# Kernel optimization log

Measured on AMD Instinct MI355X. Metric: run time of the kernel, lower is better.

## Reference

```python
import jax, jax.numpy as jnp
import numpy as np


def setup_inputs() -> dict:
    key = jax.random.key(0)
    k1, k2 = jax.random.split(key)
    B, S, D, K = 8, 2048, 512, 8192
    x = jax.random.normal(k1, (B, S, D), dtype=jnp.float32)
    codebook = jax.random.normal(k2, (K, D), dtype=jnp.float32)
    return {"x": x, "codebook": codebook}


def reference(x, codebook):
    # x: [B, S, D], codebook: [K, D]
    B, S, D = x.shape
    flat_x = x.reshape(-1, D)                      # [N, D], N = B*S
    distances = (
        jnp.sum(flat_x * flat_x, axis=1, keepdims=True)
        - 2.0 * jnp.matmul(flat_x, codebook.T)
        + jnp.sum(codebook * codebook, axis=1)
    )
    encoding_indices = jnp.argmin(distances, axis=1)  # [N]
    quantized = codebook[encoding_indices]            # [N, D] embedding lookup
    return quantized.reshape(x.shape)                 # [B, S, D]
```

## Files before the change

### kernel.cpp

```cpp
#include <hip/hip_runtime.h>


#define MROWS 16384
#define KCB   8192
#define DDIM  512
#define BM 256
#define BN 256
#define BK 64
#define NKT (DDIM / BK)
#define NTILES (KCB / 128)
#define MARGIN 8.0f

typedef unsigned short u16;
typedef unsigned int uint;
typedef __attribute__((ext_vector_type(8))) short bf16x8;
typedef __attribute__((ext_vector_type(4))) float f32x4;

__device__ inline u16 f2bf(float f) {
  unsigned int u = __float_as_uint(f);
  u += 0x7FFFu + ((u >> 16) & 1u);
  return (u16)(u >> 16);
}

__device__ inline void gload16(const void* g, void* l) {
  __builtin_amdgcn_global_load_lds((const __attribute__((address_space(1))) void*)g,
                                   (__attribute__((address_space(3))) void*)l,
                                   16, 0, 0);
}

__device__ inline double shfl_xor_dbl(double v, int m) {
  long long l = __double_as_longlong(v);
  int lo = (int)(l & 0xffffffffLL), hi = (int)(l >> 32);
  lo = __shfl_xor(lo, m, 64);
  hi = __shfl_xor(hi, m, 64);
  return __longlong_as_double(((long long)hi << 32) | (unsigned long long)(unsigned int)lo);
}

__device__ inline float keyval(uint k) {
  uint u = k & 0xFFFFFF80u;
  uint bits = (u & 0x80000000u) ? (u & 0x7FFFFFFFu) : ~u;
  return __uint_as_float(bits);
}


__global__ __launch_bounds__(256) void k_conv_x(const float* __restrict__ x,
                                                u16* __restrict__ xb) {
  size_t i = ((size_t)blockIdx.x * 256 + threadIdx.x) * 8;
  float4 a = *(const float4*)(x + i);
  float4 b = *(const float4*)(x + i + 4);
  union { u16 s[8]; uint4 v; } u;
  u.s[0]=f2bf(a.x); u.s[1]=f2bf(a.y); u.s[2]=f2bf(a.z); u.s[3]=f2bf(a.w);
  u.s[4]=f2bf(b.x); u.s[5]=f2bf(b.y); u.s[6]=f2bf(b.z); u.s[7]=f2bf(b.w);
  *(uint4*)(xb + i) = u.v;
}

__global__ __launch_bounds__(256) void k_conv_cb(const float* __restrict__ cb,
                                                 u16* __restrict__ cbb,
                                                 float* __restrict__ cnorm) {
  int k = blockIdx.x * 4 + (threadIdx.x >> 6);
  int lane = threadIdx.x & 63;
  size_t base = (size_t)k * DDIM + lane * 8;
  float4 a = *(const float4*)(cb + base);
  float4 b = *(const float4*)(cb + base + 4);
  union { u16 s[8]; uint4 v; } u;
  u.s[0]=f2bf(a.x); u.s[1]=f2bf(a.y); u.s[2]=f2bf(a.z); u.s[3]=f2bf(a.w);
  u.s[4]=f2bf(b.x); u.s[5]=f2bf(b.y); u.s[6]=f2bf(b.z); u.s[7]=f2bf(b.w);
  *(uint4*)(cbb + base) = u.v;
  float s = a.x*a.x + a.y*a.y + a.z*a.z + a.w*a.w
          + b.x*b.x + b.y*b.y + b.z*b.z + b.w*b.w;
  #pragma unroll
  for (int m = 1; m < 64; m <<= 1) s += __shfl_xor(s, m, 64);
  if (lane == 0) cnorm[k] = s;
}


__global__ __launch_bounds__(512, 2) void k_gemm_min(
    const u16* __restrict__ Xbf, const u16* __restrict__ Cbf,
    const float* __restrict__ cnorm, uint2* __restrict__ stats)
{
  extern __shared__ u16 lds[];

  int bid = blockIdx.x;
  int xcd = bid & 7;
  int j   = bid >> 3;
  int mTile = xcd * 8 + (j & 7);
  int nTile = j >> 3;
  int rowBase = mTile * BM;
  int colBase = nTile * BN;

  int tid = threadIdx.x;
  int lane = tid & 63;
  int wv = tid >> 6;
  int wr = wv >> 2;
  int wc = wv & 3;
  int grp = lane >> 4;
  int l15 = lane & 15;

  const u16 *srcX[4], *srcC[4];
  #pragma unroll
  for (int i = 0; i < 4; ++i) {
    int f = i * 512 + tid;
    int r = f >> 3;
    int p = f & 7;
    int gc = (p ^ (r & 7)) << 3;
    srcX[i] = Xbf + (size_t)(rowBase + r) * DDIM + gc;
    srcC[i] = Cbf + (size_t)(colBase + r) * DDIM + gc;
  }

  f32x4 acc[8][4];
  #pragma unroll
  for (int mi = 0; mi < 8; ++mi)
    #pragma unroll
    for (int ni = 0; ni < 4; ++ni)
      acc[mi][ni] = (f32x4){0.f, 0.f, 0.f, 0.f};

#define STAGE(cur_, kt_)                                                     \
  {                                                                          \
    u16* Xd = lds + (cur_) * 16384;                                          \
    u16* Cd = lds + 32768 + (cur_) * 16384;                                  \
    _Pragma("unroll")                                                        \
    for (int i = 0; i < 4; ++i) {                                            \
      gload16(srcX[i] + (kt_) * BK, (void*)(Xd + (i * 512 + wv * 64) * 8));  \
      gload16(srcC[i] + (kt_) * BK, (void*)(Cd + (i * 512 + wv * 64) * 8));  \
    }                                                                        \
  }

  STAGE(0, 0);
  STAGE(1, 1);
  __syncthreads();

  int cur = 0;
  for (int kt = 0; kt < NKT; ++kt) {
    const u16* Xb = lds + cur * 16384;
    const u16* Cs = lds + 32768 + cur * 16384;
    #pragma unroll
    for (int ks = 0; ks < 2; ++ks) {
      bf16x8 xF[4];
      #pragma unroll
      for (int ni = 0; ni < 4; ++ni) {
        int rX = wc * 64 + ni * 16 + l15;
        xF[ni] = *(const bf16x8*)&Xb[rX * BK + (((ks * 4 + grp) ^ (rX & 7)) << 3)];
      }
      #pragma unroll
      for (int mi = 0; mi < 8; ++mi) {
        int rC = wr * 128 + mi * 16 + l15;
        bf16x8 cF = *(const bf16x8*)&Cs[rC * BK + (((ks * 4 + grp) ^ (rC & 7)) << 3)];
        #pragma unroll
        for (int ni = 0; ni < 4; ++ni)
          acc[mi][ni] = __builtin_amdgcn_mfma_f32_16x16x32_bf16(cF, xF[ni], acc[mi][ni], 0, 0, 0);
      }
    }
    __syncthreads();
    if (kt + 2 < NKT) STAGE(cur, kt + 2);
    cur ^= 1;
  }
#undef STAGE

#define INS(st1, st2, st3, kx)                                     \
  { uint kk_ = (kx);                                               \
    bool lt1 = kk_ < st1, lt2 = kk_ < st2, lt3 = kk_ < st3;        \
    st3 = lt3 ? (lt2 ? st2 : kk_) : st3;                           \
    st2 = lt2 ? (lt1 ? st1 : kk_) : st2;                           \
    st1 = lt1 ? kk_ : st1; }

  uint t1[4], t2[4], t3[4];
  #pragma unroll
  for (int ni = 0; ni < 4; ++ni) { t1[ni] = 0xFFFFFFFFu; t2[ni] = 0xFFFFFFFFu; t3[ni] = 0xFFFFFFFFu; }

  #pragma unroll
  for (int mi = 0; mi < 8; ++mi) {
    float cnv[4];
    *(float4*)cnv = *(const float4*)&cnorm[colBase + wr * 128 + mi * 16 + grp * 4];
    #pragma unroll
    for (int ni = 0; ni < 4; ++ni) {
      #pragma unroll
      for (int rg = 0; rg < 4; ++rg) {
        float v = cnv[rg] - 2.0f * acc[mi][ni][rg];
        uint u = __float_as_uint(v);
        u = ((int)u < 0) ? ~u : (u | 0x80000000u);
        uint key = (u & 0xFFFFFF80u) | (uint)(mi * 16 + grp * 4 + rg);
        INS(t1[ni], t2[ni], t3[ni], key);
      }
    }
  }
  #pragma unroll
  for (int ni = 0; ni < 4; ++ni) {
    #pragma unroll
    for (int mk = 16; mk <= 32; mk <<= 1) {
      uint o1 = (uint)__shfl_xor((int)t1[ni], mk, 64);
      uint o2 = (uint)__shfl_xor((int)t2[ni], mk, 64);
      uint o3 = (uint)__shfl_xor((int)t3[ni], mk, 64);
      INS(t1[ni], t2[ni], t3[ni], o1);
      INS(t1[ni], t2[ni], t3[ni], o2);
      INS(t1[ni], t2[ni], t3[ni], o3);
    }
  }
#undef INS
  if (grp == 0) {
    #pragma unroll
    for (int ni = 0; ni < 4; ++ni) {
      float v1 = keyval(t1[ni]), v2 = keyval(t2[ni]), v3 = keyval(t3[ni]);
      uint i1 = t1[ni] & 127u, i2 = t2[ni] & 127u;
      uint d2 = min(255u, (uint)((v2 - v1) * 4.0f));
      uint d3 = min(255u, (uint)((v3 - v1) * 4.0f));
      uint2 st;
      st.x = __float_as_uint(v1);
      st.y = i1 | (i2 << 7) | (d2 << 14) | (d3 << 22);
      int xrow = rowBase + wc * 64 + ni * 16 + l15;
      stats[(size_t)xrow * NTILES + nTile * 2 + wr] = st;
    }
  }
}


__device__ inline void eval64(const float4& xa, const float4& xb,
                              const float* __restrict__ cb, int col,
                              double& best, int& bi, int lane) {
  const float* cr = cb + (size_t)col * DDIM + lane * 8;
  float4 ca = *(const float4*)cr;
  float4 cv = *(const float4*)(cr + 4);
  double s = 0.0, d;
  d = (double)xa.x - (double)ca.x; s += d*d;
  d = (double)xa.y - (double)ca.y; s += d*d;
  d = (double)xa.z - (double)ca.z; s += d*d;
  d = (double)xa.w - (double)ca.w; s += d*d;
  d = (double)xb.x - (double)cv.x; s += d*d;
  d = (double)xb.y - (double)cv.y; s += d*d;
  d = (double)xb.z - (double)cv.z; s += d*d;
  d = (double)xb.w - (double)cv.w; s += d*d;
  #pragma unroll
  for (int m = 1; m < 64; m <<= 1) s += shfl_xor_dbl(s, m);
  if (s < best || (s == best && col < bi)) { best = s; bi = col; }
}

__global__ __launch_bounds__(256) void k_refine(
    const float* __restrict__ x, const float* __restrict__ cb,
    const float* __restrict__ cnorm, const uint2* __restrict__ stats,
    unsigned int* __restrict__ bestOut)
{
  int n = blockIdx.x * 4 + (threadIdx.x >> 6);
  int lane = threadIdx.x & 63;
  uint2 st = stats[(size_t)n * NTILES + lane];
  float m1 = __uint_as_float(st.x);
  int   i1 = st.y & 127, i2 = (st.y >> 7) & 127;
  float m2 = m1 + ((st.y >> 14) & 255u) * 0.25f;
  float m3 = m1 + ((st.y >> 22) & 255u) * 0.25f;
  float g = m1;
  #pragma unroll
  for (int m = 1; m < 64; m <<= 1) g = fminf(g, __shfl_xor(g, m, 64));
  float T = g + MARGIN;
  unsigned long long q1 = __ballot(m1 <= T);
  unsigned long long q2 = __ballot(m2 <= T);
  unsigned long long qr = __ballot(m3 <= T);

  const float* xr = x + (size_t)n * DDIM;
  float4 xa = *(const float4*)(xr + lane * 8);
  float4 xb = *(const float4*)(xr + lane * 8 + 4);

  double best = 1e300;
  int bi = 0x7fffffff;

  while (q1) {
    int t = __ffsll(q1) - 1; q1 &= q1 - 1;
    int col = t * 128 + __shfl(i1, t, 64);
    eval64(xa, xb, cb, col, best, bi, lane);
  }
  while (q2) {
    int t = __ffsll(q2) - 1; q2 &= q2 - 1;
    int col = t * 128 + __shfl(i2, t, 64);
    eval64(xa, xb, cb, col, best, bi, lane);
  }
  while (qr) {
    int t = __ffsll(qr) - 1; qr &= qr - 1;
    for (int c2 = 0; c2 < 128; ++c2) {
      int col2 = t * 128 + c2;
      const float* cr = cb + (size_t)col2 * DDIM + lane * 8;
      float4 ca = *(const float4*)cr;
      float4 cv = *(const float4*)(cr + 4);
      float p = xa.x*ca.x + xa.y*ca.y + xa.z*ca.z + xa.w*ca.w
              + xb.x*cv.x + xb.y*cv.y + xb.z*cv.z + xb.w*cv.w;
      #pragma unroll
      for (int m = 1; m < 64; m <<= 1) p += __shfl_xor(p, m, 64);
      float s32 = cnorm[col2] - 2.0f * p;
      if (s32 <= T) {
        double s = 0.0, dd;
        dd = (double)xa.x - (double)ca.x; s += dd*dd;
        dd = (double)xa.y - (double)ca.y; s += dd*dd;
        dd = (double)xa.z - (double)ca.z; s += dd*dd;
        dd = (double)xa.w - (double)ca.w; s += dd*dd;
        dd = (double)xb.x - (double)cv.x; s += dd*dd;
        dd = (double)xb.y - (double)cv.y; s += dd*dd;
        dd = (double)xb.z - (double)cv.z; s += dd*dd;
        dd = (double)xb.w - (double)cv.w; s += dd*dd;
        #pragma unroll
        for (int m = 1; m < 64; m <<= 1) s += shfl_xor_dbl(s, m);
        if (s < best || (s == best && col2 < bi)) { best = s; bi = col2; }
      }
    }
  }
  if (lane == 0) bestOut[n] = (unsigned int)bi;
}


__global__ __launch_bounds__(256) void k_gather(const float* __restrict__ cb,
                                                const unsigned int* __restrict__ bestIdx,
                                                float* __restrict__ out) {
  int n = blockIdx.x * 4 + (threadIdx.x >> 6);
  int lane = threadIdx.x & 63;
  unsigned int b = bestIdx[n];
  const float4* s = (const float4*)(cb + (size_t)b * DDIM);
  float4* dp = (float4*)(out + (size_t)n * DDIM);
  dp[lane * 2]     = s[lane * 2];
  dp[lane * 2 + 1] = s[lane * 2 + 1];
}


extern "C" void kernel_launch(void* const* d_in, const int* in_sizes, int n_in,
                              void* d_out, int out_size, void* d_ws, size_t ws_size,
                              hipStream_t stream) {
  const float* x  = (const float*)d_in[0];
  const float* cb = (const float*)d_in[1];
  float* out = (float*)d_out;

  char* ob = (char*)d_out;
  u16*   Xbf   = (u16*)ob;
  u16*   Cbf   = (u16*)(ob + 16ull * 1024 * 1024);
  uint2* stats = (uint2*)(ob + 24ull * 1024 * 1024);

  char* wsb = (char*)d_ws;
  float* cnorm = (float*)wsb;
  unsigned int* bestIdx = (unsigned int*)(wsb + 32 * 1024);

  (void)hipFuncSetAttribute((const void*)k_gemm_min,
                            hipFuncAttributeMaxDynamicSharedMemorySize, 131072);

  k_conv_x  <<<4096, 256, 0, stream>>>(x, Xbf);
  k_conv_cb <<<2048, 256, 0, stream>>>(cb, Cbf, cnorm);
  k_gemm_min<<<2048, 512, 131072, stream>>>(Xbf, Cbf, cnorm, stats);
  k_refine  <<<4096, 256, 0, stream>>>(x, cb, cnorm, stats, bestIdx);
  k_gather  <<<4096, 256, 0, stream>>>(cb, bestIdx, out);
}
```

Before: 267.6 us.

## Restructure GEMM main loop into fine-grained phased pipeline with manual waitcnt

Replaces the double-buffered K-loop (two syncthreads per tile) with an eight-phase schedule per pair of K-tiles. Each phase loads a quarter of the next tile's operands with direct-to-LDS loads, waits on vmcnt by hand, and issues 16 MFMAs at raised wave priority. The LDS layout is split into half-tiles and offsets are precomputed. The goal is finer overlap of global loads, LDS reads and MFMA work, at the cost of fragile hand-written barrier and waitcnt logic that could introduce races.

```diff
diff --git a/kernel.cpp b/kernel.cpp
--- a/kernel.cpp
+++ b/kernel.cpp
@@ -4,10 +4,7 @@
 #define MROWS 16384
 #define KCB   8192
 #define DDIM  512
-#define BM 256
-#define BN 256
-#define BK 64
-#define NKT (DDIM / BK)
+#define NKT   8
 #define NTILES (KCB / 128)
 #define MARGIN 8.0f
 
@@ -78,15 +75,15 @@
     const u16* __restrict__ Xbf, const u16* __restrict__ Cbf,
     const float* __restrict__ cnorm, uint2* __restrict__ stats)
 {
-  extern __shared__ u16 lds[];
+  extern __shared__ __align__(16) u16 lds[];
 
   int bid = blockIdx.x;
   int xcd = bid & 7;
   int j   = bid >> 3;
   int mTile = xcd * 8 + (j & 7);
   int nTile = j >> 3;
-  int rowBase = mTile * BM;
-  int colBase = nTile * BN;
+  int rowBase = mTile * 256;
+  int colBase = nTile * 256;
 
   int tid = threadIdx.x;
   int lane = tid & 63;
@@ -96,16 +93,18 @@
   int grp = lane >> 4;
   int l15 = lane & 15;
 
-  const u16 *srcX[4], *srcC[4];
-  #pragma unroll
-  for (int i = 0; i < 4; ++i) {
-    int f = i * 512 + tid;
-    int r = f >> 3;
-    int p = f & 7;
-    int gc = (p ^ (r & 7)) << 3;
-    srcX[i] = Xbf + (size_t)(rowBase + r) * DDIM + gc;
-    srcC[i] = Cbf + (size_t)(colBase + r) * DDIM + gc;
-  }
+  const int rr = tid >> 3;
+  const int pc = (tid & 7) ^ (rr & 7);
+  const u16* pA = Cbf + (size_t)(colBase + rr) * DDIM + pc * 8;
+  const u16* pB = Xbf + (size_t)(rowBase + rr) * DDIM + pc * 8;
+
+  const int m7 = l15 & 7;
+  const int ch0 = (grp ^ m7);
+  const int ch1 = ch0 ^ 4;
+  const int cOff0 = wr * 4096 + l15 * 64 + ch0 * 8;
+  const int cOff1 = wr * 4096 + l15 * 64 + ch1 * 8;
+  const int xOff0 = wc * 4096 + l15 * 64 + ch0 * 8;
+  const int xOff1 = wc * 4096 + l15 * 64 + ch1 * 8;
 
   f32x4 acc[8][4];
   #pragma unroll
@@ -114,47 +113,72 @@
     for (int ni = 0; ni < 4; ++ni)
       acc[mi][ni] = (f32x4){0.f, 0.f, 0.f, 0.f};
 
-#define STAGE(cur_, kt_)                                                     \
-  {                                                                          \
-    u16* Xd = lds + (cur_) * 16384;                                          \
-    u16* Cd = lds + 32768 + (cur_) * 16384;                                  \
-    _Pragma("unroll")                                                        \
-    for (int i = 0; i < 4; ++i) {                                            \
-      gload16(srcX[i] + (kt_) * BK, (void*)(Xd + (i * 512 + wv * 64) * 8));  \
-      gload16(srcC[i] + (kt_) * BK, (void*)(Cd + (i * 512 + wv * 64) * 8));  \
-    }                                                                        \
-  }
-
-  STAGE(0, 0);
-  STAGE(1, 1);
-  __syncthreads();
-
-  int cur = 0;
-  for (int kt = 0; kt < NKT; ++kt) {
-    const u16* Xb = lds + cur * 16384;
-    const u16* Cs = lds + 32768 + cur * 16384;
-    #pragma unroll
-    for (int ks = 0; ks < 2; ++ks) {
-      bf16x8 xF[4];
+  gload16(pB,           (void*)&lds[32768 + tid * 8]);
+  gload16(pB + 32768,   (void*)&lds[32768 + 4096 + tid * 8]);
+  gload16(pB + 65536,   (void*)&lds[32768 + 8192 + tid * 8]);
+  gload16(pB + 98304,   (void*)&lds[32768 + 12288 + tid * 8]);
+  gload16(pA,           (void*)&lds[tid * 8]);
+  gload16(pA + 65536,   (void*)&lds[4096 + tid * 8]);
+  gload16(pA + 32768,   (void*)&lds[8192 + tid * 8]);
+  gload16(pA + 98304,   (void*)&lds[8192 + 4096 + tid * 8]);
+
+  bf16x8 xF[4];
+
+  #pragma unroll
+  for (int it = 0; it < 4; ++it) {
+    #pragma unroll
+    for (int ph = 0; ph < 8; ++ph) {
+      const int b  = ph >> 2;
+      const int s  = ph & 3;
+      const int h  = s & 1;
+      const int ks = s >> 1;
+      const int tauS = 2 * it + 1 + (ph >> 2);
+      const int bS = (ph < 4) ? 1 : 0;
+
+      if ((ph & 2) == 0) {
+        if (it == 3 && ph == 5) { asm volatile("s_waitcnt vmcnt(0)" ::: "memory"); }
+        else                    { asm volatile("s_waitcnt vmcnt(2)" ::: "memory"); }
+      }
+      __builtin_amdgcn_s_barrier();
+      __builtin_amdgcn_sched_barrier(0);
+
+      bf16x8 cF[4];
       #pragma unroll
-      for (int ni = 0; ni < 4; ++ni) {
-        int rX = wc * 64 + ni * 16 + l15;
-        xF[ni] = *(const bf16x8*)&Xb[rX * BK + (((ks * 4 + grp) ^ (rX & 7)) << 3)];
-      }
-      #pragma unroll
-      for (int mi = 0; mi < 8; ++mi) {
-        int rC = wr * 128 + mi * 16 + l15;
-        bf16x8 cF = *(const bf16x8*)&Cs[rC * BK + (((ks * 4 + grp) ^ (rC & 7)) << 3)];
+      for (int q = 0; q < 4; ++q)
+        cF[q] = *(const bf16x8*)&lds[b * 16384 + h * 8192 + q * 1024 + (ks ? cOff1 : cOff0)];
+      if (h == 0) {
         #pragma unroll
         for (int ni = 0; ni < 4; ++ni)
-          acc[mi][ni] = __builtin_amdgcn_mfma_f32_16x16x32_bf16(cF, xF[ni], acc[mi][ni], 0, 0, 0);
-      }
-    }
-    __syncthreads();
-    if (kt + 2 < NKT) STAGE(cur, kt + 2);
-    cur ^= 1;
-  }
-#undef STAGE
+          xF[ni] = *(const bf16x8*)&lds[32768 + b * 16384 + ni * 1024 + (ks ? xOff1 : xOff0)];
+      }
+
+      if (!(it == 3 && ph >= 4)) {
+        if (s < 2) {
+          gload16(pB + s * 65536 + tauS * 64,
+                  (void*)&lds[32768 + bS * 16384 + s * 8192 + tid * 8]);
+          gload16(pB + s * 65536 + 32768 + tauS * 64,
+                  (void*)&lds[32768 + bS * 16384 + s * 8192 + 4096 + tid * 8]);
+        } else {
+          const int ha = s - 2;
+          gload16(pA + ha * 32768 + tauS * 64,
+                  (void*)&lds[bS * 16384 + ha * 8192 + tid * 8]);
+          gload16(pA + ha * 32768 + 65536 + tauS * 64,
+                  (void*)&lds[bS * 16384 + ha * 8192 + 4096 + tid * 8]);
+        }
+      }
+
+      asm volatile("s_waitcnt lgkmcnt(0)" ::: "memory");
+      __builtin_amdgcn_sched_barrier(0);
+      __builtin_amdgcn_s_setprio(1);
+      #pragma unroll
+      for (int q = 0; q < 4; ++q)
+        #pragma unroll
+        for (int ni = 0; ni < 4; ++ni)
+          acc[h * 4 + q][ni] =
+            __builtin_amdgcn_mfma_f32_16x16x32_bf16(cF[q], xF[ni], acc[h * 4 + q][ni], 0, 0, 0);
+      __builtin_amdgcn_s_setprio(0);
+    }
+  }
 
 #define INS(st1, st2, st3, kx)                                     \
   { uint kk_ = (kx);                                               \
```

New measurement: 257.4 us. 3.8% less time.

## Shrink GEMM tile to 128x256 with BK32, raise occupancy, fuse refine+gather

Applied to the files above, without the earlier changes.

Retiles the bf16 distance GEMM from 256x256 with BK=64 to 128 rows by 256 codewords with BK=32. Per-block LDS drops from 128KB to 48KB, so four 512-thread blocks can fit per CU, and wave priority is raised around the MFMA burst. A new LDS cross-wave merge combines the two 64-codeword halves into the existing per-128-column top-3 stats. When the workspace is large enough, stats move to the workspace and refine and gather fuse into one kernel, saving a launch and the index round trip. The smaller tile lowers data reuse per loaded byte and adds a synchronised merge step.

```diff
diff --git a/kernel.cpp b/kernel.cpp
--- a/kernel.cpp
+++ b/kernel.cpp
@@ -4,11 +4,8 @@
 #define MROWS 16384
 #define KCB   8192
 #define DDIM  512
-#define BM 256
-#define BN 256
-#define BK 64
-#define NKT (DDIM / BK)
-#define NTILES (KCB / 128)
+#define NKT   16
+#define NTILES 64
 #define MARGIN 8.0f
 
 typedef unsigned short u16;
@@ -74,55 +71,55 @@
 }
 
 
-__global__ __launch_bounds__(512, 2) void k_gemm_min(
+__global__ __launch_bounds__(512, 4) void k_gemm_min(
     const u16* __restrict__ Xbf, const u16* __restrict__ Cbf,
     const float* __restrict__ cnorm, uint2* __restrict__ stats)
 {
-  extern __shared__ u16 lds[];
+  extern __shared__ __align__(16) u16 lds[];
 
   int bid = blockIdx.x;
   int xcd = bid & 7;
   int j   = bid >> 3;
-  int mTile = xcd * 8 + (j & 7);
-  int nTile = j >> 3;
-  int rowBase = mTile * BM;
-  int colBase = nTile * BN;
+  int mTile = xcd * 16 + (j & 15);
+  int nTile = j >> 4;
+  int rowBase = mTile * 128;
+  int colBase = nTile * 256;
 
   int tid = threadIdx.x;
   int lane = tid & 63;
   int wv = tid >> 6;
-  int wr = wv >> 2;
-  int wc = wv & 3;
+  int wr = wv & 3;
+  int wc = wv >> 2;
   int grp = lane >> 4;
   int l15 = lane & 15;
 
-  const u16 *srcX[4], *srcC[4];
+  const int ar = tid >> 2;
+  const int ac = ((tid & 3) ^ ((ar + (ar >> 2)) & 3)) << 3;
+  const u16* pA = Cbf + (size_t)(colBase + ar) * DDIM + ac;
+  const u16* pB = Xbf + (size_t)(rowBase + ar) * DDIM + ac;
+
+  int offA[4], offX[4];
   #pragma unroll
   for (int i = 0; i < 4; ++i) {
-    int f = i * 512 + tid;
-    int r = f >> 3;
-    int p = f & 7;
-    int gc = (p ^ (r & 7)) << 3;
-    srcX[i] = Xbf + (size_t)(rowBase + r) * DDIM + gc;
-    srcC[i] = Cbf + (size_t)(colBase + r) * DDIM + gc;
-  }
-
-  f32x4 acc[8][4];
-  #pragma unroll
-  for (int mi = 0; mi < 8; ++mi)
+    int rA = wr * 64 + i * 16 + l15;
+    offA[i] = rA * 32 + ((grp ^ ((rA + (rA >> 2)) & 3)) << 3);
+    int rX = wc * 64 + i * 16 + l15;
+    offX[i] = 8192 + rX * 32 + ((grp ^ ((rX + (rX >> 2)) & 3)) << 3);
+  }
+
+  f32x4 acc[4][4];
+  #pragma unroll
+  for (int mi = 0; mi < 4; ++mi)
     #pragma unroll
     for (int ni = 0; ni < 4; ++ni)
       acc[mi][ni] = (f32x4){0.f, 0.f, 0.f, 0.f};
 
-#define STAGE(cur_, kt_)                                                     \
-  {                                                                          \
-    u16* Xd = lds + (cur_) * 16384;                                          \
-    u16* Cd = lds + 32768 + (cur_) * 16384;                                  \
-    _Pragma("unroll")                                                        \
-    for (int i = 0; i < 4; ++i) {                                            \
-      gload16(srcX[i] + (kt_) * BK, (void*)(Xd + (i * 512 + wv * 64) * 8));  \
-      gload16(srcC[i] + (kt_) * BK, (void*)(Cd + (i * 512 + wv * 64) * 8));  \
-    }                                                                        \
+#define STAGE(b_, T)                                                          \
+  {                                                                           \
+    u16* Ad = lds + (b_) * 12288;                                             \
+    gload16(pA + (T) * 32,               (void*)(Ad + tid * 8));              \
+    gload16(pA + 65536 + (T) * 32,       (void*)(Ad + 4096 + tid * 8));       \
+    gload16(pB + (T) * 32,               (void*)(Ad + 8192 + tid * 8));       \
   }
 
   STAGE(0, 0);
@@ -131,25 +128,19 @@
 
   int cur = 0;
   for (int kt = 0; kt < NKT; ++kt) {
-    const u16* Xb = lds + cur * 16384;
-    const u16* Cs = lds + 32768 + cur * 16384;
-    #pragma unroll
-    for (int ks = 0; ks < 2; ++ks) {
-      bf16x8 xF[4];
+    const u16* base = lds + cur * 12288;
+    bf16x8 cF[4], xF[4];
+    #pragma unroll
+    for (int mi = 0; mi < 4; ++mi) cF[mi] = *(const bf16x8*)&base[offA[mi]];
+    #pragma unroll
+    for (int ni = 0; ni < 4; ++ni) xF[ni] = *(const bf16x8*)&base[offX[ni]];
+    __builtin_amdgcn_s_setprio(1);
+    #pragma unroll
+    for (int mi = 0; mi < 4; ++mi)
       #pragma unroll
-      for (int ni = 0; ni < 4; ++ni) {
-        int rX = wc * 64 + ni * 16 + l15;
-        xF[ni] = *(const bf16x8*)&Xb[rX * BK + (((ks * 4 + grp) ^ (rX & 7)) << 3)];
-      }
-      #pragma unroll
-      for (int mi = 0; mi < 8; ++mi) {
-        int rC = wr * 128 + mi * 16 + l15;
-        bf16x8 cF = *(const bf16x8*)&Cs[rC * BK + (((ks * 4 + grp) ^ (rC & 7)) << 3)];
-        #pragma unroll
-        for (int ni = 0; ni < 4; ++ni)
-          acc[mi][ni] = __builtin_amdgcn_mfma_f32_16x16x32_bf16(cF, xF[ni], acc[mi][ni], 0, 0, 0);
-      }
-    }
+      for (int ni = 0; ni < 4; ++ni)
+        acc[mi][ni] = __builtin_amdgcn_mfma_f32_16x16x32_bf16(cF[mi], xF[ni], acc[mi][ni], 0, 0, 0);
+    __builtin_amdgcn_s_setprio(0);
     __syncthreads();
     if (kt + 2 < NKT) STAGE(cur, kt + 2);
     cur ^= 1;
@@ -167,10 +158,11 @@
   #pragma unroll
   for (int ni = 0; ni < 4; ++ni) { t1[ni] = 0xFFFFFFFFu; t2[ni] = 0xFFFFFFFFu; t3[ni] = 0xFFFFFFFFu; }
 
-  #pragma unroll
-  for (int mi = 0; mi < 8; ++mi) {
+  const uint tagBase = (uint)((wr & 1) * 64);
+  #pragma unroll
+  for (int mi = 0; mi < 4; ++mi) {
     float cnv[4];
-    *(float4*)cnv = *(const float4*)&cnorm[colBase + wr * 128 + mi * 16 + grp * 4];
+    *(float4*)cnv = *(const float4*)&cnorm[colBase + wr * 64 + mi * 16 + grp * 4];
     #pragma unroll
     for (int ni = 0; ni < 4; ++ni) {
       #pragma unroll
@@ -178,7 +170,7 @@
         float v = cnv[rg] - 2.0f * acc[mi][ni][rg];
         uint u = __float_as_uint(v);
         u = ((int)u < 0) ? ~u : (u | 0x80000000u);
-        uint key = (u & 0xFFFFFF80u) | (uint)(mi * 16 + grp * 4 + rg);
+        uint key = (u & 0xFFFFFF80u) | (tagBase + (uint)(mi * 16 + grp * 4 + rg));
         INS(t1[ni], t2[ni], t3[ni], key);
       }
     }
@@ -195,21 +187,35 @@
       INS(t1[ni], t2[ni], t3[ni], o3);
     }
   }
+
+  uint* scK = (uint*)lds;
+  if (grp == 0) {
+    #pragma unroll
+    for (int ni = 0; ni < 4; ++ni) {
+      int xloc = wc * 64 + ni * 16 + l15;
+      uint* p = &scK[(wr * 128 + xloc) * 3];
+      p[0] = t1[ni]; p[1] = t2[ni]; p[2] = t3[ni];
+    }
+  }
+  __syncthreads();
+  if (tid < 256) {
+    int xr = tid & 127;
+    int s  = tid >> 7;
+    const uint* pa = &scK[((2 * s) * 128 + xr) * 3];
+    const uint* pb = &scK[((2 * s + 1) * 128 + xr) * 3];
+    uint a1 = pa[0], a2 = pa[1], a3 = pa[2];
+    #pragma unroll
+    for (int z = 0; z < 3; ++z) INS(a1, a2, a3, pb[z]);
+    float v1 = keyval(a1), v2 = keyval(a2), v3 = keyval(a3);
+    uint i1 = a1 & 127u, i2 = a2 & 127u;
+    uint d2 = min(255u, (uint)((v2 - v1) * 4.0f));
+    uint d3 = min(255u, (uint)((v3 - v1) * 4.0f));
+    uint2 st;
+    st.x = __float_as_uint(v1);
+    st.y = i1 | (i2 << 7) | (d2 << 14) | (d3 << 22);
+    stats[(size_t)(rowBase + xr) * NTILES + nTile * 2 + s] = st;
+  }
 #undef INS
-  if (grp == 0) {
-    #pragma unroll
-    for (int ni = 0; ni < 4; ++ni) {
-      float v1 = keyval(t1[ni]), v2 = keyval(t2[ni]), v3 = keyval(t3[ni]);
-      uint i1 = t1[ni] & 127u, i2 = t2[ni] & 127u;
-      uint d2 = min(255u, (uint)((v2 - v1) * 4.0f));
-      uint d3 = min(255u, (uint)((v3 - v1) * 4.0f));
-      uint2 st;
-      st.x = __float_as_uint(v1);
-      st.y = i1 | (i2 << 7) | (d2 << 14) | (d3 << 22);
-      int xrow = rowBase + wc * 64 + ni * 16 + l15;
-      stats[(size_t)xrow * NTILES + nTile * 2 + wr] = st;
-    }
-  }
 }
 
 
@@ -233,13 +239,10 @@
   if (s < best || (s == best && col < bi)) { best = s; bi = col; }
 }
 
-__global__ __launch_bounds__(256) void k_refine(
-    const float* __restrict__ x, const float* __restrict__ cb,
-    const float* __restrict__ cnorm, const uint2* __restrict__ stats,
-    unsigned int* __restrict__ bestOut)
-{
-  int n = blockIdx.x * 4 + (threadIdx.x >> 6);
-  int lane = threadIdx.x & 63;
+__device__ inline int refine_row(int n, int lane,
+                                 const float* __restrict__ x, const float* __restrict__ cb,
+                                 const float* __restrict__ cnorm,
+                                 const uint2* __restrict__ stats) {
   uint2 st = stats[(size_t)n * NTILES + lane];
   float m1 = __uint_as_float(st.x);
   int   i1 = st.y & 127, i2 = (st.y >> 7) & 127;
@@ -298,9 +301,33 @@
       }
     }
   }
+  return bi;
+}
+
+__global__ __launch_bounds__(256) void k_refine(
+    const float* __restrict__ x, const float* __restrict__ cb,
+    const float* __restrict__ cnorm, const uint2* __restrict__ stats,
+    unsigned int* __restrict__ bestOut)
+{
+  int n = blockIdx.x * 4 + (threadIdx.x >> 6);
+  int lane = threadIdx.x & 63;
+  int bi = refine_row(n, lane, x, cb, cnorm, stats);
   if (lane == 0) bestOut[n] = (unsigned int)bi;
 }
 
+__global__ __launch_bounds__(256) void k_refine_gather(
+    const float* __restrict__ x, const float* __restrict__ cb,
+    const float* __restrict__ cnorm, const uint2* __restrict__ stats,
+    float* __restrict__ out)
+{
+  int n = blockIdx.x * 4 + (threadIdx.x >> 6);
+  int lane = threadIdx.x & 63;
+  int bi = refine_row(n, lane, x, cb, cnorm, stats);
+  const float4* s = (const float4*)(cb + (size_t)bi * DDIM);
+  float4* dp = (float4*)(out + (size_t)n * DDIM);
+  dp[lane * 2]     = s[lane * 2];
+  dp[lane * 2 + 1] = s[lane * 2 + 1];
+}
 
 __global__ __launch_bounds__(256) void k_gather(const float* __restrict__ cb,
                                                 const unsigned int* __restrict__ bestIdx,
@@ -323,20 +350,28 @@
   float* out = (float*)d_out;
 
   char* ob = (char*)d_out;
-  u16*   Xbf   = (u16*)ob;
-  u16*   Cbf   = (u16*)(ob + 16ull * 1024 * 1024);
-  uint2* stats = (uint2*)(ob + 24ull * 1024 * 1024);
+  u16* Xbf = (u16*)ob;
+  u16* Cbf = (u16*)(ob + 16ull * 1024 * 1024);
 
   char* wsb = (char*)d_ws;
   float* cnorm = (float*)wsb;
   unsigned int* bestIdx = (unsigned int*)(wsb + 32 * 1024);
 
+  const size_t statsBytes = (size_t)MROWS * NTILES * sizeof(uint2);
+  bool fuse = ws_size >= 96 * 1024 + statsBytes;
+  uint2* stats = fuse ? (uint2*)(wsb + 96 * 1024)
+                      : (uint2*)(ob + 24ull * 1024 * 1024);
+
   (void)hipFuncSetAttribute((const void*)k_gemm_min,
-                            hipFuncAttributeMaxDynamicSharedMemorySize, 131072);
+                            hipFuncAttributeMaxDynamicSharedMemorySize, 49152);
 
   k_conv_x  <<<4096, 256, 0, stream>>>(x, Xbf);
   k_conv_cb <<<2048, 256, 0, stream>>>(cb, Cbf, cnorm);
-  k_gemm_min<<<2048, 512, 131072, stream>>>(Xbf, Cbf, cnorm, stats);
-  k_refine  <<<4096, 256, 0, stream>>>(x, cb, cnorm, stats, bestIdx);
-  k_gather  <<<4096, 256, 0, stream>>>(cb, bestIdx, out);
-}
+  k_gemm_min<<<4096, 512, 49152, stream>>>(Xbf, Cbf, cnorm, stats);
+  if (fuse) {
+    k_refine_gather<<<4096, 256, 0, stream>>>(x, cb, cnorm, stats, out);
+  } else {
+    k_refine<<<4096, 256, 0, stream>>>(x, cb, cnorm, stats, bestIdx);
+    k_gather<<<4096, 256, 0, stream>>>(cb, bestIdx, out);
+  }
+}
```

Result: faster. 252.7 us (-5.6%).
